# Kernel tuning notes

Hardware: AMD Instinct MI355X
Metric: run time of the kernel (lower is better)

Reference implementation:

```python
import jax, jax.numpy as jnp
import numpy as np
import math

DIM = 1024
NUM_HEADS = 16
HEAD_DIM = DIM // NUM_HEADS
EPS = 1e-6
DILATED = 2
WINDOW = 2  # window_size init arg; actual window = L * WINDOW per side


def setup_inputs() -> dict:
    key = jax.random.key(0)
    ks = jax.random.split(key, 14)
    B, S = 1, 8704
    x = jax.random.normal(ks[0], (B, S, DIM), jnp.float32)
    ang = jax.random.uniform(ks[1], (S, HEAD_DIM // 2), jnp.float32, -jnp.pi, jnp.pi)
    freqs_cos = jnp.cos(ang)
    freqs_sin = jnp.sin(ang)
    def lin(k):
        return 0.02 * jax.random.normal(k, (DIM, DIM), jnp.float32)
    def bias(k):
        return 0.01 * jax.random.normal(k, (DIM,), jnp.float32)
    return {
        'x': x, 'freqs_cos': freqs_cos, 'freqs_sin': freqs_sin,
        'wq': lin(ks[2]), 'bq': bias(ks[3]),
        'wk': lin(ks[4]), 'bk': bias(ks[5]),
        'wv': lin(ks[6]), 'bv': bias(ks[7]),
        'wo': lin(ks[8]), 'bo': bias(ks[9]),
        'gq': 1.0 + 0.02 * jax.random.normal(ks[10], (DIM,), jnp.float32),
        'gk': 1.0 + 0.02 * jax.random.normal(ks[11], (DIM,), jnp.float32),
        'f': 34, 'L': 256,
    }


def rmsnorm(h, g):
    return h * jax.lax.rsqrt(jnp.mean(h * h, axis=-1, keepdims=True) + EPS) * g


def rope(h, cos, sin):
    # h: [B,S,D] viewed as interleaved complex pairs per head, rotated by unit freqs
    B, S, D = h.shape
    hp = h.reshape(B, S, NUM_HEADS, HEAD_DIM // 2, 2)
    a, b = hp[..., 0], hp[..., 1]
    c = cos[None, :, None, :]
    s = sin[None, :, None, :]
    ra = a * c - b * s
    rb = a * s + b * c
    return jnp.stack([ra, rb], axis=-1).reshape(B, S, D)


def windowed_attention(q, k, v, w):
    # sliding-window attention: query i attends keys j with |i-j| <= w (inclusive)
    B, S, D = q.shape
    H, hd = NUM_HEADS, HEAD_DIM
    def heads(t):
        return t.reshape(B, S, H, hd).transpose(0, 2, 1, 3)  # [B,H,S,hd]
    qh, kh, vh = heads(q), heads(k), heads(v)
    C = w  # block size == window -> only 3 neighbor key blocks per query block
    pad = (-S) % C
    Sp = S + pad
    nb = Sp // C
    def blocks(t):
        return jnp.pad(t, ((0, 0), (0, 0), (0, pad), (0, 0))).reshape(B, H, nb, C, hd)
    qb = blocks(qh)
    def win(t):
        tb = jnp.pad(blocks(t), ((0, 0), (0, 0), (1, 1), (0, 0), (0, 0)))
        return jnp.concatenate([tb[:, :, i:i + nb] for i in range(3)], axis=3)  # [B,H,nb,3C,hd]
    kw_, vw_ = win(kh), win(vh)
    scores = jnp.einsum('bhnqd,bhnkd->bhnqk', qb, kw_) * (1.0 / math.sqrt(hd))
    qi = jnp.arange(nb)[:, None, None] * C + jnp.arange(C)[None, :, None]      # [nb,C,1]
    kj = (jnp.arange(nb)[:, None, None] - 1) * C + jnp.arange(3 * C)[None, None, :]  # [nb,1,3C]
    valid = (kj >= 0) & (kj < S) & (qi - kj <= w) & (kj - qi <= w)
    scores = jnp.where(valid, scores, -1e9)
    p = jax.nn.softmax(scores, axis=-1)
    o = jnp.einsum('bhnqk,bhnkd->bhnqd', p, vw_)
    return o.reshape(B, H, Sp, hd)[:, :, :S].transpose(0, 2, 1, 3).reshape(B, S, D)


def reference(x, freqs_cos, freqs_sin, wq, bq, wk, bk, wv, bv, wo, bo, gq, gk, f, L):
    B, S, D = x.shape
    q = rope(rmsnorm(x @ wq + bq, gq), freqs_cos, freqs_sin)
    k = rope(rmsnorm(x @ wk + bk, gk), freqs_cos, freqs_sin)
    v = x @ wv + bv
    w = L * WINDOW
    use_dilated = DILATED > 1 and S // (DILATED * L) > 1
    if use_dilated:
        blk = DILATED * L
        pad_len = blk - S % blk  # == blk when S % blk == 0 (faithful to torch code)
        Sp = S + pad_len
        n = Sp // blk
        def padd(t):
            return jnp.pad(t, ((0, 0), (0, pad_len), (0, 0)))
        def dil(t):
            # 'b (n d l) c -> (b d) (n l) c'
            return t.reshape(B, n, DILATED, L, D).transpose(0, 2, 1, 3, 4).reshape(B * DILATED, n * L, D)
        q, k, v = dil(padd(q)), dil(padd(k)), dil(padd(v))
    o = windowed_attention(q, k, v, w)
    out = o @ wo + bo
    if use_dilated:
        # '(b d) (n l) c -> b (n d l) c', then drop pad
        out = out.reshape(B, DILATED, n, L, D).transpose(0, 2, 1, 3, 4).reshape(B, n * DILATED * L, D)
        out = out[:, :S]
    return out
```

## Files before the change

### kernel.cpp

```cpp
#include <hip/hip_runtime.h>
#include <hip/hip_bf16.h>
#include <stdint.h>

#define DIM 1024
#define NH 16
#define HD 64
#define S_ORIG 8704
#define WIN 512

typedef __attribute__((ext_vector_type(8))) short short8;
typedef __attribute__((ext_vector_type(4))) float f32x4;

__device__ __forceinline__ float bf2f(unsigned short u) {
    return __uint_as_float(((unsigned int)u) << 16);
}
__device__ __forceinline__ unsigned short f2bf(float f) {
    unsigned int x = __float_as_uint(f);
    unsigned int r = x + 0x7fffu + ((x >> 16) & 1u);
    return (unsigned short)(r >> 16);
}
__device__ __forceinline__ unsigned int pkbf(float a, float b) {
    unsigned int ua = (__float_as_uint(a) + 0x8000u) >> 16;
    unsigned int ub = (__float_as_uint(b) + 0x8000u) & 0xffff0000u;
    return ua | ub;
}

#define GLD_LDS(gptr, lptr) \
    __builtin_amdgcn_global_load_lds((const __attribute__((address_space(1))) void*)(gptr), \
                                     (__attribute__((address_space(3))) void*)(lptr), 16, 0, 0)

__global__ __launch_bounds__(256) void prep(const float* __restrict__ x,
                                            unsigned short* __restrict__ xb,
                                            const float* __restrict__ w0,
                                            const float* __restrict__ w1,
                                            const float* __restrict__ w2,
                                            const float* __restrict__ w3,
                                            unsigned short* __restrict__ wt) {
    __shared__ float ts[64][65];
    const int bx = blockIdx.x;
    const int t = threadIdx.x;
    if (bx < 8704) {
        int i = (bx * 256 + t) * 4;
        float4 v = *(const float4*)(x + i);
        ushort4 o;
        o.x = f2bf(v.x); o.y = f2bf(v.y); o.z = f2bf(v.z); o.w = f2bf(v.w);
        *(ushort4*)(xb + i) = o;
        return;
    }
    const int b = bx - 8704;
    const int z = b >> 8;
    const int rem = b & 255;
    const int kb = (rem >> 4) * 64, nb = (rem & 15) * 64;
    const float* w = z == 0 ? w0 : z == 1 ? w1 : z == 2 ? w2 : w3;
    unsigned short* o = wt + (size_t)z * DIM * DIM;
    const int c = t & 63, r4 = t >> 6;
#pragma unroll
    for (int rr = 0; rr < 16; rr++) {
        int row = rr * 4 + r4;
        ts[row][c] = w[(size_t)(kb + row) * DIM + nb + c];
    }
    __syncthreads();
#pragma unroll
    for (int rr = 0; rr < 16; rr++) {
        int nl = rr * 4 + r4;
        o[(size_t)(nb + nl) * DIM + kb + c] = f2bf(ts[c][nl]);
    }
}

template <int OUTF32>
__global__ __launch_bounds__(256) void gemm_bf16(const unsigned short* __restrict__ A,
                                                 const unsigned short* __restrict__ Bt,
                                                 const float* __restrict__ b0,
                                                 const float* __restrict__ b1,
                                                 const float* __restrict__ b2,
                                                 void* __restrict__ Cout) {
    __shared__ __align__(16) unsigned short As[128 * 64];
    __shared__ __align__(16) unsigned short Bs[128 * 64];
    const int z = blockIdx.z;
    const unsigned short* B = Bt + (size_t)z * DIM * DIM;
    const float* bias = z == 0 ? b0 : (z == 1 ? b1 : b2);
    const int m0 = blockIdx.y * 128, n0 = blockIdx.x * 128;
    const int tid = threadIdx.x;
    const int lane = tid & 63, wv = tid >> 6;
    const int wr = wv >> 1, wc = wv & 1;
    const int quad = lane >> 4, r = lane & 15;

    f32x4 acc[4][4];
#pragma unroll
    for (int i = 0; i < 4; i++)
#pragma unroll
        for (int j = 0; j < 4; j++)
#pragma unroll
            for (int t4 = 0; t4 < 4; t4++) acc[i][j][t4] = 0.0f;

    const unsigned short* a_base = A + (size_t)m0 * DIM;
    const unsigned short* b_base = B + (size_t)n0 * DIM;
    int st_row[4], st_gc[4];
#pragma unroll
    for (int i = 0; i < 4; i++) {
        const int c = wv * 256 + i * 64 + lane;
        st_row[i] = c >> 3;
        st_gc[i] = ((c & 7) ^ (st_row[i] & 7)) * 8;
    }

    for (int k0 = 0; k0 < DIM; k0 += 64) {
        __syncthreads();
#pragma unroll
        for (int i = 0; i < 4; i++) {
            GLD_LDS(a_base + (size_t)st_row[i] * DIM + k0 + st_gc[i], &As[(wv * 256 + i * 64) * 8]);
            GLD_LDS(b_base + (size_t)st_row[i] * DIM + k0 + st_gc[i], &Bs[(wv * 256 + i * 64) * 8]);
        }
        __syncthreads();
#pragma unroll
        for (int kh = 0; kh < 2; kh++) {
            short8 af[4], bfr[4];
#pragma unroll
            for (int i = 0; i < 4; i++) {
                const int row = wr * 64 + i * 16 + r;
                const int pc = ((quad + 4 * kh) ^ (row & 7)) * 8;
                af[i] = *(const short8*)&As[row * 64 + pc];
            }
#pragma unroll
            for (int j = 0; j < 4; j++) {
                const int row = wc * 64 + j * 16 + r;
                const int pc = ((quad + 4 * kh) ^ (row & 7)) * 8;
                bfr[j] = *(const short8*)&Bs[row * 64 + pc];
            }
#pragma unroll
            for (int i = 0; i < 4; i++)
#pragma unroll
                for (int j = 0; j < 4; j++)
                    acc[i][j] = __builtin_amdgcn_mfma_f32_16x16x32_bf16(af[i], bfr[j], acc[i][j], 0, 0, 0);
        }
    }

#pragma unroll
    for (int i = 0; i < 4; i++) {
        const int row = m0 + wr * 64 + i * 16 + quad * 4;
#pragma unroll
        for (int j = 0; j < 4; j++) {
            const int col = n0 + wc * 64 + j * 16 + r;
            const float bvl = bias[col];
#pragma unroll
            for (int t4 = 0; t4 < 4; t4++) {
                float vv = acc[i][j][t4] + bvl;
                if (OUTF32) {
                    ((float*)Cout)[(size_t)(row + t4) * DIM + col] = vv;
                } else {
                    ((unsigned short*)Cout)[(size_t)z * S_ORIG * DIM + (size_t)(row + t4) * DIM + col] = f2bf(vv);
                }
            }
        }
    }
}

__global__ __launch_bounds__(256) void norm_rope(unsigned short* __restrict__ hq,
                                                 unsigned short* __restrict__ hk,
                                                 const float* __restrict__ gq,
                                                 const float* __restrict__ gk,
                                                 const float* __restrict__ fcos,
                                                 const float* __restrict__ fsin) {
    const int z = blockIdx.y;
    unsigned short* h = z == 0 ? hq : hk;
    const float* g = z == 0 ? gq : gk;
    const int w = threadIdx.x >> 6, lane = threadIdx.x & 63;
    const int srow = blockIdx.x * 4 + w;
    unsigned short* hp = h + (size_t)srow * DIM;
    const int p0 = lane * 8, p1 = 512 + lane * 8;

    union { int4 i4; unsigned short u[8]; } r0, r1, o0, o1;
    r0.i4 = *(const int4*)(hp + p0);
    r1.i4 = *(const int4*)(hp + p1);
    float v[16];
#pragma unroll
    for (int j = 0; j < 8; j++) { v[j] = bf2f(r0.u[j]); v[8 + j] = bf2f(r1.u[j]); }

    float ss = 0.0f;
#pragma unroll
    for (int j = 0; j < 16; j++) ss += v[j] * v[j];
#pragma unroll
    for (int off = 1; off < 64; off <<= 1) ss += __shfl_xor(ss, off, 64);
    const float rinv = rsqrtf(ss * (1.0f / DIM) + 1e-6f);

    float4 ga = *(const float4*)(g + p0), gb = *(const float4*)(g + p0 + 4);
    float4 gc = *(const float4*)(g + p1), gd = *(const float4*)(g + p1 + 4);
    const float* gg[4] = {&ga.x, &gb.x, &gc.x, &gd.x};
#pragma unroll
    for (int q4 = 0; q4 < 4; q4++)
#pragma unroll
        for (int j = 0; j < 4; j++) v[q4 * 4 + j] *= rinv * gg[q4][j];

    const int i0 = (p0 & 63) >> 1;
    float4 cs = *(const float4*)(fcos + (size_t)srow * 32 + i0);
    float4 sn = *(const float4*)(fsin + (size_t)srow * 32 + i0);
    const float* cp = &cs.x;
    const float* sp = &sn.x;
#pragma unroll
    for (int seg = 0; seg < 2; seg++) {
        unsigned short* uo = seg == 0 ? o0.u : o1.u;
#pragma unroll
        for (int pr = 0; pr < 4; pr++) {
            const float a = v[seg * 8 + pr * 2], b = v[seg * 8 + pr * 2 + 1];
            uo[pr * 2]     = f2bf(a * cp[pr] - b * sp[pr]);
            uo[pr * 2 + 1] = f2bf(a * sp[pr] + b * cp[pr]);
        }
    }
    *(int4*)(hp + p0) = o0.i4;
    *(int4*)(hp + p1) = o1.i4;
}

__global__ __launch_bounds__(256) void attn(const unsigned short* __restrict__ qkv,
                                            unsigned short* __restrict__ ob) {
    __shared__ __align__(16) unsigned short Ks[64 * 72];
    __shared__ __align__(16) unsigned short Vt[64 * 72];
    __shared__ __align__(16) unsigned short Ps[4][16 * 72];

    const int head = blockIdx.x >> 1;
    const int d = blockIdx.x & 1;
    const int qt = blockIdx.y;
    const int tid = threadIdx.x;
    const int lane = tid & 63, wv = tid >> 6;
    const int quad = lane >> 4, r16 = lane & 15;

    const unsigned short* qb = qkv;
    const unsigned short* kb = qkv + (size_t)S_ORIG * DIM;
    const unsigned short* vb = qkv + (size_t)2 * S_ORIG * DIM;

    const int qi = qt * 64 + wv * 16 + r16;
    const int og_q = ((qi >> 8) << 9) + d * 256 + (qi & 255);
    short8 qf[2];
    {
        const unsigned short* qrow = qb + (size_t)og_q * DIM + head * HD + quad * 8;
#pragma unroll
        for (int c = 0; c < 2; c++) {
            union { int4 i4; unsigned short u[8]; short8 s8; } in, outv;
            in.i4 = *(const int4*)(qrow + c * 32);
#pragma unroll
            for (int j = 0; j < 8; j++) outv.u[j] = f2bf(bf2f(in.u[j]) * 0.18033688f);
            qf[c] = outv.s8;
        }
    }

    f32x4 oacc[4];
    float lsum = 0.0f;
#pragma unroll
    for (int nt = 0; nt < 4; nt++)
#pragma unroll
        for (int rr = 0; rr < 4; rr++) oacc[nt][rr] = 0.0f;

    const int kt_lo = (qt - 8 > 0) ? (qt - 8) : 0;
    const int kt_hi = (qt + 8 < 67) ? (qt + 8) : 67;

    const int st_row0 = tid >> 3, st_ch = (tid & 7) * 8;
    const int vt_kk = (tid & 31) * 2, vt_d0 = (tid >> 5) * 8;

    for (int kt = kt_lo; kt <= kt_hi; kt++) {
        const int kbase = kt * 64;
        __syncthreads();

#pragma unroll
        for (int half = 0; half < 2; half++) {
            const int row = st_row0 + half * 32;
            const int kj = kbase + row;
            const int ok = ((kj >> 8) << 9) + d * 256 + (kj & 255);
            *(int4*)&Ks[row * 72 + st_ch] = *(const int4*)(kb + (size_t)ok * DIM + head * HD + st_ch);
        }
        {
            const int kj0 = kbase + vt_kk;
            const int ok0 = ((kj0 >> 8) << 9) + d * 256 + (kj0 & 255);
            union { int4 i4; unsigned short u[8]; } a0, a1;
            a0.i4 = *(const int4*)(vb + (size_t)ok0 * DIM + head * HD + vt_d0);
            a1.i4 = *(const int4*)(vb + (size_t)(ok0 + 1) * DIM + head * HD + vt_d0);
#pragma unroll
            for (int i = 0; i < 8; i++) {
                unsigned int pack = (unsigned int)a0.u[i] | ((unsigned int)a1.u[i] << 16);
                *(unsigned int*)&Vt[(vt_d0 + i) * 72 + vt_kk] = pack;
            }
        }
        __syncthreads();

        f32x4 sv[4];
#pragma unroll
        for (int nt = 0; nt < 4; nt++) {
            short8 k0f = *(const short8*)&Ks[(nt * 16 + r16) * 72 + quad * 8];
            short8 k1f = *(const short8*)&Ks[(nt * 16 + r16) * 72 + 32 + quad * 8];
            f32x4 a = {0.0f, 0.0f, 0.0f, 0.0f};
            a = __builtin_amdgcn_mfma_f32_16x16x32_bf16(k0f, qf[0], a, 0, 0, 0);
            a = __builtin_amdgcn_mfma_f32_16x16x32_bf16(k1f, qf[1], a, 0, 0, 0);
            sv[nt] = a;
        }

        const bool edge = (kt == qt - 8) || (kt == qt + 8);
        unsigned short* pw = &Ps[wv][0];
#pragma unroll
        for (int nt = 0; nt < 4; nt++) {
            float p[4];
#pragma unroll
            for (int rr = 0; rr < 4; rr++) {
                float e = exp2f(sv[nt][rr]);
                if (edge) {
                    const int kj = kbase + nt * 16 + quad * 4 + rr;
                    const int dl = qi - kj;
                    if (dl > WIN || dl < -WIN) e = 0.0f;
                }
                p[rr] = e;
            }
            lsum += (p[0] + p[1]) + (p[2] + p[3]);
            uint2 pk;
            pk.x = pkbf(p[0], p[1]);
            pk.y = pkbf(p[2], p[3]);
            *(uint2*)&pw[r16 * 72 + nt * 16 + quad * 4] = pk;
        }
        __asm__ volatile("s_waitcnt lgkmcnt(0)" ::: "memory");

        short8 pf0 = *(const short8*)&pw[r16 * 72 + quad * 8];
        short8 pf1 = *(const short8*)&pw[r16 * 72 + 32 + quad * 8];
#pragma unroll
        for (int nt = 0; nt < 4; nt++) {
            short8 v0f = *(const short8*)&Vt[(nt * 16 + r16) * 72 + quad * 8];
            short8 v1f = *(const short8*)&Vt[(nt * 16 + r16) * 72 + 32 + quad * 8];
            oacc[nt] = __builtin_amdgcn_mfma_f32_16x16x32_bf16(v0f, pf0, oacc[nt], 0, 0, 0);
            oacc[nt] = __builtin_amdgcn_mfma_f32_16x16x32_bf16(v1f, pf1, oacc[nt], 0, 0, 0);
        }
    }

    lsum += __shfl_xor(lsum, 16, 64);
    lsum += __shfl_xor(lsum, 32, 64);
    {
        const int cnt = (qi + WIN < 4607 ? qi + WIN : 4607) - 4351;
        if (cnt > 0) lsum += (float)cnt;
    }
    const float linv = 1.0f / lsum;

#pragma unroll
    for (int nt = 0; nt < 4; nt++) {
        ushort4 o;
        o.x = f2bf(oacc[nt][0] * linv);
        o.y = f2bf(oacc[nt][1] * linv);
        o.z = f2bf(oacc[nt][2] * linv);
        o.w = f2bf(oacc[nt][3] * linv);
        *(ushort4*)&ob[(size_t)og_q * DIM + head * HD + nt * 16 + quad * 4] = o;
    }
}

extern "C" void kernel_launch(void* const* d_in, const int* in_sizes, int n_in,
                              void* d_out, int out_size, void* d_ws, size_t ws_size,
                              hipStream_t stream) {
    const float* x    = (const float*)d_in[0];
    const float* fcos = (const float*)d_in[1];
    const float* fsin = (const float*)d_in[2];
    const float* wq   = (const float*)d_in[3];
    const float* bq   = (const float*)d_in[4];
    const float* wk   = (const float*)d_in[5];
    const float* bk   = (const float*)d_in[6];
    const float* wv   = (const float*)d_in[7];
    const float* bv   = (const float*)d_in[8];
    const float* wo   = (const float*)d_in[9];
    const float* bo   = (const float*)d_in[10];
    const float* gq   = (const float*)d_in[11];
    const float* gk   = (const float*)d_in[12];

    char* ws = (char*)d_ws;
    unsigned short* xb = (unsigned short*)(ws);
    unsigned short* wt = (unsigned short*)(ws + 17825792);
    unsigned short* h  = (unsigned short*)(ws + 26214400);
    unsigned short* ob = (unsigned short*)(ws + 79691776);
    float* outp = (float*)d_out;

    prep<<<9728, 256, 0, stream>>>(x, xb, wq, wk, wv, wo, wt);
    gemm_bf16<0><<<dim3(8, 68, 3), 256, 0, stream>>>(xb, wt, bq, bk, bv, (void*)h);
    norm_rope<<<dim3(2176, 2), 256, 0, stream>>>(h, h + (size_t)S_ORIG * DIM, gq, gk, fcos, fsin);
    attn<<<dim3(32, 68), 256, 0, stream>>>(h, ob);
    gemm_bf16<1><<<dim3(8, 68, 1), 256, 0, stream>>>(ob, wt + (size_t)3 * DIM * DIM, bo, bo, bo, (void*)outp);
}
```

Before: 339.9 us.

## Replace direct-to-LDS GEMM loads with register-staged K=32 tiles; switch softmax to __expf

The GEMM drops global_load_lds and instead loads 32-wide K slices into registers, then stores them to swizzled LDS. This halves LDS usage and doubles the number of K iterations and barriers. The idea is that prefetching into registers before the barrier lets global loads overlap the previous compute. Separately, the attention kernel now scales q by 1/8 and uses __expf instead of pre-scaling by log2e and calling exp2f, which is mathematically equivalent.

```diff
diff --git a/kernel.cpp b/kernel.cpp
--- a/kernel.cpp
+++ b/kernel.cpp
@@ -24,10 +24,6 @@
     unsigned int ub = (__float_as_uint(b) + 0x8000u) & 0xffff0000u;
     return ua | ub;
 }
-
-#define GLD_LDS(gptr, lptr) \
-    __builtin_amdgcn_global_load_lds((const __attribute__((address_space(1))) void*)(gptr), \
-                                     (__attribute__((address_space(3))) void*)(lptr), 16, 0, 0)
 
 __global__ __launch_bounds__(256) void prep(const float* __restrict__ x,
                                             unsigned short* __restrict__ xb,
@@ -74,8 +70,8 @@
                                                  const float* __restrict__ b1,
                                                  const float* __restrict__ b2,
                                                  void* __restrict__ Cout) {
-    __shared__ __align__(16) unsigned short As[128 * 64];
-    __shared__ __align__(16) unsigned short Bs[128 * 64];
+    __shared__ __align__(16) unsigned short As[128 * 32];
+    __shared__ __align__(16) unsigned short Bs[128 * 32];
     const int z = blockIdx.z;
     const unsigned short* B = Bt + (size_t)z * DIM * DIM;
     const float* bias = z == 0 ? b0 : (z == 1 ? b1 : b2);
@@ -95,43 +91,34 @@
 
     const unsigned short* a_base = A + (size_t)m0 * DIM;
     const unsigned short* b_base = B + (size_t)n0 * DIM;
-    int st_row[4], st_gc[4];
-#pragma unroll
-    for (int i = 0; i < 4; i++) {
-        const int c = wv * 256 + i * 64 + lane;
-        st_row[i] = c >> 3;
-        st_gc[i] = ((c & 7) ^ (st_row[i] & 7)) * 8;
-    }
-
-    for (int k0 = 0; k0 < DIM; k0 += 64) {
+    const int c0 = tid, c1 = 256 + tid;
+    const int r0 = c0 >> 2, o0 = (((c0 & 3) ^ ((c0 >> 3) & 3))) * 8;
+    const int r1 = c1 >> 2, o1 = (((c1 & 3) ^ ((c1 >> 3) & 3))) * 8;
+    const int jsw = (quad ^ ((r >> 1) & 3)) * 8;
+
+    for (int k0 = 0; k0 < DIM; k0 += 32) {
+        int4 a0 = *(const int4*)(a_base + (size_t)r0 * DIM + k0 + o0);
+        int4 a1 = *(const int4*)(a_base + (size_t)r1 * DIM + k0 + o1);
+        int4 g0 = *(const int4*)(b_base + (size_t)r0 * DIM + k0 + o0);
+        int4 g1 = *(const int4*)(b_base + (size_t)r1 * DIM + k0 + o1);
         __syncthreads();
-#pragma unroll
-        for (int i = 0; i < 4; i++) {
-            GLD_LDS(a_base + (size_t)st_row[i] * DIM + k0 + st_gc[i], &As[(wv * 256 + i * 64) * 8]);
-            GLD_LDS(b_base + (size_t)st_row[i] * DIM + k0 + st_gc[i], &Bs[(wv * 256 + i * 64) * 8]);
-        }
+        *(int4*)&As[c0 * 8] = a0;
+        *(int4*)&As[c1 * 8] = a1;
+        *(int4*)&Bs[c0 * 8] = g0;
+        *(int4*)&Bs[c1 * 8] = g1;
         __syncthreads();
-#pragma unroll
-        for (int kh = 0; kh < 2; kh++) {
-            short8 af[4], bfr[4];
-#pragma unroll
-            for (int i = 0; i < 4; i++) {
-                const int row = wr * 64 + i * 16 + r;
-                const int pc = ((quad + 4 * kh) ^ (row & 7)) * 8;
-                af[i] = *(const short8*)&As[row * 64 + pc];
-            }
-#pragma unroll
-            for (int j = 0; j < 4; j++) {
-                const int row = wc * 64 + j * 16 + r;
-                const int pc = ((quad + 4 * kh) ^ (row & 7)) * 8;
-                bfr[j] = *(const short8*)&Bs[row * 64 + pc];
-            }
-#pragma unroll
-            for (int i = 0; i < 4; i++)
-#pragma unroll
-                for (int j = 0; j < 4; j++)
-                    acc[i][j] = __builtin_amdgcn_mfma_f32_16x16x32_bf16(af[i], bfr[j], acc[i][j], 0, 0, 0);
-        }
+        short8 af[4], bfr[4];
+#pragma unroll
+        for (int i = 0; i < 4; i++)
+            af[i] = *(const short8*)&As[(wr * 64 + i * 16 + r) * 32 + jsw];
+#pragma unroll
+        for (int j = 0; j < 4; j++)
+            bfr[j] = *(const short8*)&Bs[(wc * 64 + j * 16 + r) * 32 + jsw];
+#pragma unroll
+        for (int i = 0; i < 4; i++)
+#pragma unroll
+            for (int j = 0; j < 4; j++)
+                acc[i][j] = __builtin_amdgcn_mfma_f32_16x16x32_bf16(af[i], bfr[j], acc[i][j], 0, 0, 0);
     }
 
 #pragma unroll
@@ -236,7 +223,7 @@
             union { int4 i4; unsigned short u[8]; short8 s8; } in, outv;
             in.i4 = *(const int4*)(qrow + c * 32);
 #pragma unroll
-            for (int j = 0; j < 8; j++) outv.u[j] = f2bf(bf2f(in.u[j]) * 0.18033688f);
+            for (int j = 0; j < 8; j++) outv.u[j] = f2bf(bf2f(in.u[j]) * 0.125f);
             qf[c] = outv.s8;
         }
     }
@@ -297,7 +284,7 @@
             float p[4];
 #pragma unroll
             for (int rr = 0; rr < 4; rr++) {
-                float e = exp2f(sv[nt][rr]);
+                float e = __expf(sv[nt][rr]);
                 if (edge) {
                     const int kj = kbase + nt * 16 + quad * 4 + rr;
                     const int dl = qi - kj;
```

New measurement: 352.2 us. +3.6%, slower.
